# Kernel tuning notes

Measured on AMD Instinct MI355X. Metric: run time of the kernel, lower is better.

Reference implementation:

```python
import jax, jax.numpy as jnp
import numpy as np

B, S, D, H, FF = 2, 2048, 1024, 16, 4096
HD = D // H
EPS = 1e-9


def setup_inputs() -> dict:
    key = jax.random.key(0)
    ks = jax.random.split(key, 16)
    sc = 0.02
    inp = {
        "x": jax.random.normal(ks[0], (B, S, D), jnp.float32),
        "y": jax.random.normal(ks[1], (B, S, D), jnp.float32),
        "decoder_mask": jnp.tril(jnp.ones((S, S), jnp.int32))[None, None],  # [1,1,S,S]
        # self-attention params (weights stored [in,out])
        "qkv_w": jax.random.normal(ks[2], (D, 3 * D), jnp.float32) * sc,
        "qkv_b": jnp.zeros((3 * D,), jnp.float32),
        "sa_fc_w": jax.random.normal(ks[3], (D, D), jnp.float32) * sc,
        "sa_fc_b": jnp.zeros((D,), jnp.float32),
        "g1": jnp.ones((D,), jnp.float32),
        "b1": jnp.zeros((D,), jnp.float32),
        # cross-attention params
        "kv_w": jax.random.normal(ks[4], (D, 2 * D), jnp.float32) * sc,
        "kv_b": jnp.zeros((2 * D,), jnp.float32),
        "q_w": jax.random.normal(ks[5], (D, D), jnp.float32) * sc,
        "q_b": jnp.zeros((D,), jnp.float32),
        "ca_fc_w": jax.random.normal(ks[6], (D, D), jnp.float32) * sc,
        "ca_fc_b": jnp.zeros((D,), jnp.float32),
        "g2": jnp.ones((D,), jnp.float32),
        "b2": jnp.zeros((D,), jnp.float32),
        # FFN params
        "ff1_w": jax.random.normal(ks[7], (D, FF), jnp.float32) * sc,
        "ff1_b": jnp.zeros((FF,), jnp.float32),
        "ff2_w": jax.random.normal(ks[8], (FF, D), jnp.float32) * sc,
        "ff2_b": jnp.zeros((D,), jnp.float32),
        "g3": jnp.ones((D,), jnp.float32),
        "b3": jnp.zeros((D,), jnp.float32),
    }
    return inp


def _layernorm(x, g, b):
    mean = jnp.mean(x, axis=-1, keepdims=True)
    var = jnp.mean((x - mean) ** 2, axis=-1, keepdims=True)
    return g * (x - mean) / jnp.sqrt(var + EPS) + b


def _sdpa(q, k, v, mask=None):
    # q,k,v: [B,H,S,hd]
    scores = jnp.einsum("bhqd,bhkd->bhqk", q, k) / jnp.sqrt(jnp.float32(q.shape[-1]))
    if mask is not None:
        scores = jnp.where(mask == 0, jnp.float32(-1e9), scores)
    attn = jax.nn.softmax(scores, axis=-1)
    return jnp.einsum("bhqk,bhkd->bhqd", attn, v)


def reference(x, y, decoder_mask, qkv_w, qkv_b, sa_fc_w, sa_fc_b, g1, b1,
              kv_w, kv_b, q_w, q_b, ca_fc_w, ca_fc_b, g2, b2,
              ff1_w, ff1_b, ff2_w, ff2_b, g3, b3):
    b, s, d = y.shape
    # --- masked self-attention on y ---
    qkv = (y @ qkv_w + qkv_b).reshape(b, s, H, 3 * HD).transpose(0, 2, 1, 3)
    q, k, v = jnp.split(qkv, 3, axis=-1)
    vals = _sdpa(q, k, v, decoder_mask).transpose(0, 2, 1, 3).reshape(b, s, d)
    sa = vals @ sa_fc_w + sa_fc_b
    y = _layernorm(sa + y, g1, b1)
    # --- cross-attention: kv from x, q from y ---
    kv = (x @ kv_w + kv_b).reshape(b, s, H, 2 * HD).transpose(0, 2, 1, 3)
    k2, v2 = jnp.split(kv, 2, axis=-1)
    q2 = (y @ q_w + q_b).reshape(b, s, H, HD).transpose(0, 2, 1, 3)
    vals2 = _sdpa(q2, k2, v2, None).transpose(0, 2, 1, 3).reshape(b, s, d)
    ca = vals2 @ ca_fc_w + ca_fc_b
    y = _layernorm(ca + y, g2, b2)
    # --- FFN ---
    h = jax.nn.relu(y @ ff1_w + ff1_b)
    ff = h @ ff2_w + ff2_b
    y = _layernorm(ff + y, g3, b3)
    return y
```

## Files before the change

### kernel.cpp

```cpp
#include <hip/hip_runtime.h>

typedef unsigned short u16;
typedef unsigned int u32;
typedef __attribute__((ext_vector_type(4))) float f32x4;
typedef __attribute__((ext_vector_type(8))) __bf16 bf16x8;
typedef __attribute__((ext_vector_type(2))) __bf16 bf16x2;
typedef __attribute__((ext_vector_type(4))) u16 u16x4;

#define NB 2
#define NS 2048
#define ND 1024
#define NH 16
#define NHD 64
#define NFF 4096
#define NBS (NB * NS)

typedef const __attribute__((address_space(1))) unsigned int as1_u32;
typedef __attribute__((address_space(3))) unsigned int as3_u32;

__device__ __forceinline__ void gl_lds16(const u16* g, u16* l) {
  __builtin_amdgcn_global_load_lds((as1_u32*)g, (as3_u32*)l, 16, 0, 0);
}

__device__ __forceinline__ u16 f2bf(float f) {
  union { float f; unsigned u; } v; v.f = f;
  unsigned r = (v.u + 0x7FFFu + ((v.u >> 16) & 1u)) >> 16;
  return (u16)r;
}

__device__ __forceinline__ float bf2f(u16 u) {
  union { u32 u; float f; } v; v.u = ((u32)u) << 16; return v.f;
}

__device__ __forceinline__ u32 pkbf(float a, float b) {
  bf16x2 v; v[0] = (__bf16)a; v[1] = (__bf16)b;
  union { bf16x2 v; u32 u; } c; c.v = v; return c.u;
}

__device__ __forceinline__ char* lswz(void* base, int row, int bcol) {
  return (char*)base + row * 128 + (bcol ^ ((row & 7) << 4));
}
__device__ __forceinline__ const char* lswz(const void* base, int row, int bcol) {
  return (const char*)base + row * 128 + (bcol ^ ((row & 7) << 4));
}

__global__ __launch_bounds__(256) void conv_bf16(const float* __restrict__ in,
                                                 u16* __restrict__ out, int n4) {
  int i = blockIdx.x * 256 + threadIdx.x;
  if (i >= n4) return;
  f32x4 v = *reinterpret_cast<const f32x4*>(&in[(size_t)i * 4]);
  u16x4 o;
#pragma unroll
  for (int j = 0; j < 4; ++j) o[j] = f2bf(v[j]);
  *reinterpret_cast<u16x4*>(&out[(size_t)i * 4]) = o;
}

struct WSeg { const float* src; u16* dst; int N; int tile0; };
struct WAll { WSeg s[7]; };

__global__ void wconv_all(WAll wa) {
  __shared__ float t[32][33];
  int bid = blockIdx.x;
  int si = 0;
#pragma unroll
  for (int i = 1; i < 7; ++i) si += (bid >= wa.s[i].tile0) ? 1 : 0;
  const WSeg sg = wa.s[si];
  const int tt = bid - sg.tile0;
  const int tilesx = sg.N >> 5;
  const int n0 = (tt % tilesx) * 32, k0 = (tt / tilesx) * 32;
  const int K = (si == 6) ? NFF : ND;
  int tx = threadIdx.x, ty = threadIdx.y;
#pragma unroll
  for (int i = ty; i < 32; i += 8) t[i][tx] = sg.src[(size_t)(k0 + i) * sg.N + n0 + tx];
  __syncthreads();
#pragma unroll
  for (int i = ty; i < 32; i += 8)
    sg.dst[(size_t)(n0 + i) * K + k0 + tx] = f2bf(t[tx][i]);
}

template <int TM, int OUTF32, int RELU>
__global__ __launch_bounds__(256) void gemm_bt(const u16* __restrict__ A,
                                               const u16* __restrict__ BT,
                                               const float* __restrict__ bias,
                                               float* __restrict__ Cf,
                                               u16* __restrict__ Cb,
                                               int M, int N, int K) {
  constexpr int MR = TM / 32;
  constexpr int ACH = TM / 64;
  __shared__ __align__(16) u16 lA[2][TM * 32];
  __shared__ __align__(16) u16 lB[2][128 * 32];
  const int tid = threadIdx.x;
  const int lane = tid & 63, wave = tid >> 6;
  const int bm = blockIdx.y * TM, bn = blockIdx.x * 128;
  const int wr = (wave >> 1) * (MR * 16), wc = (wave & 1) * 64;
  const int r16 = lane & 15, kg = lane >> 4;

  f32x4 acc[MR][4] = {};

  auto stage = [&](int buf, int k0) {
#pragma unroll
    for (int c = 0; c < ACH; ++c) {
      int chunk = c * 256 + tid;
      int r = chunk >> 2, kc = (chunk & 3) * 8;
      gl_lds16(&A[(size_t)(bm + r) * K + k0 + kc], &lA[buf][(c * 256 + wave * 64) * 8]);
    }
#pragma unroll
    for (int c = 0; c < 2; ++c) {
      int chunk = c * 256 + tid;
      int r = chunk >> 2, kc = (chunk & 3) * 8;
      gl_lds16(&BT[(size_t)(bn + r) * K + k0 + kc], &lB[buf][(c * 256 + wave * 64) * 8]);
    }
  };

  stage(0, 0);
  __syncthreads();

  const int nk = K / 32;
  for (int i = 0; i < nk; ++i) {
    const int cur = i & 1;
    if (i + 1 < nk) stage(cur ^ 1, (i + 1) * 32);

    bf16x8 af[MR], bfr[4];
#pragma unroll
    for (int m = 0; m < MR; ++m)
      af[m] = *reinterpret_cast<const bf16x8*>(&lA[cur][(wr + m * 16 + r16) * 32 + kg * 8]);
#pragma unroll
    for (int n = 0; n < 4; ++n)
      bfr[n] = *reinterpret_cast<const bf16x8*>(&lB[cur][(wc + n * 16 + r16) * 32 + kg * 8]);
#pragma unroll
    for (int m = 0; m < MR; ++m)
#pragma unroll
      for (int n = 0; n < 4; ++n)
        acc[m][n] = __builtin_amdgcn_mfma_f32_16x16x32_bf16(af[m], bfr[n], acc[m][n], 0, 0, 0);

    __syncthreads();
  }

#pragma unroll
  for (int m = 0; m < MR; ++m) {
    int row = bm + wr + m * 16 + kg * 4;
#pragma unroll
    for (int n = 0; n < 4; ++n) {
      int col = bn + wc + n * 16 + r16;
      float bv = bias[col];
#pragma unroll
      for (int j = 0; j < 4; ++j) {
        float v = acc[m][n][j] + bv;
        if (RELU) v = fmaxf(v, 0.f);
        if (OUTF32)
          Cf[(size_t)(row + j) * N + col] = v;
        else
          Cb[(size_t)(row + j) * N + col] = f2bf(v);
      }
    }
  }
}

__global__ __launch_bounds__(256) void vt_kern(const u16* __restrict__ src, int stride,
                                               int hmul, int hadd, u16* __restrict__ VT) {
  __shared__ u16 lt[64][72];
  const int bh = blockIdx.y;
  const int b = bh >> 4, h = bh & 15;
  const int s0 = blockIdx.x * 64;
  const u16* sb = src + (size_t)b * NS * stride + h * hmul + hadd;
#pragma unroll
  for (int c = 0; c < 2; ++c) {
    int chunk = c * 256 + threadIdx.x;
    int r = chunk >> 3, d = (chunk & 7) * 8;
    *reinterpret_cast<uint4*>(&lt[r][d]) =
        *reinterpret_cast<const uint4*>(&sb[(size_t)(s0 + r) * stride + d]);
  }
  __syncthreads();
  const int d = threadIdx.x >> 2, sq = (threadIdx.x & 3) * 16;
  union { u16 e[16]; uint4 v[2]; } pk;
#pragma unroll
  for (int i = 0; i < 16; ++i) pk.e[i] = lt[sq + i][d];
  uint4* dst = reinterpret_cast<uint4*>(&VT[((size_t)bh * NHD + d) * NS + s0 + sq]);
  dst[0] = pk.v[0];
  dst[1] = pk.v[1];
}

#define C1F 0.180336880f
#define OPSZ ((size_t)32 * NS * NHD)

template <int CAUSAL>
__global__ __launch_bounds__(512) void attn10(const u16* __restrict__ Qp, int qstride,
                                              int qhm, const u16* __restrict__ Kp,
                                              int kstride, int khm, int kha,
                                              const u16* __restrict__ VT,
                                              u16* __restrict__ OP,
                                              float2* __restrict__ ML) {
  const int bid = blockIdx.x;
  const int split = blockIdx.y;
  const int xcd = bid & 7, j5 = bid >> 3;
  const int bh = xcd + 8 * (j5 >> 3);
  int qt = j5 & 7;
  if (CAUSAL) qt = 7 - qt;
  const int b = bh >> 4, h = bh & 15;
  const int tid = threadIdx.x, lane = tid & 63, wave = tid >> 6;
  const int r16 = lane & 15, kg = lane >> 4;
  const int q0w = qt * 256 + wave * 32;

  __shared__ __align__(16) char lK[2][64 * 128];
  __shared__ __align__(16) char lV[2][64 * 128];
  __shared__ __align__(16) char lP[8][16 * 128];
  char* lPw = &lP[wave][0];

  const u16* qb = Qp + (size_t)b * NS * qstride + h * qhm;
  const u16* kb = Kp + (size_t)b * NS * kstride + h * khm + kha;
  const u16* vb = VT + (size_t)bh * NHD * NS;

  const int srow = tid >> 3;
  const int sbcol = (tid & 7) * 16;
  const int scol = (tid & 7) * 8;

  bf16x8 qf[2][2];
#pragma unroll
  for (int qn = 0; qn < 2; ++qn)
#pragma unroll
    for (int ks = 0; ks < 2; ++ks) {
      bf16x8 v = *reinterpret_cast<const bf16x8*>(
          &qb[(size_t)(q0w + qn * 16 + r16) * qstride + ks * 32 + kg * 8]);
#pragma unroll
      for (int e = 0; e < 8; ++e) v[e] = (__bf16)((float)v[e] * C1F);
      qf[qn][ks] = v;
    }

  f32x4 o_acc[2][4] = {};
  float m_run[2] = {-1e30f, -1e30f}, l_lane[2] = {0.f, 0.f};

  const int ntb = CAUSAL ? (4 * qt + 4) : (NS / 64);
  const int wnt = CAUSAL ? (q0w / 64 + 1) : (NS / 64);
  const int halfb = (ntb + 1) >> 1;
  const int t0 = split ? halfb : 0;
  const int t1 = split ? ntb : halfb;

  uint4 kreg, vreg;
  auto ldregs = [&](int t) {
    const int kv0 = t * 64;
    kreg = *reinterpret_cast<const uint4*>(&kb[(size_t)(kv0 + srow) * kstride + scol]);
    vreg = *reinterpret_cast<const uint4*>(&vb[(size_t)srow * NS + kv0 + scol]);
  };
  auto wrlds = [&](int buf) {
    *reinterpret_cast<uint4*>(lswz(lK[buf], srow, sbcol)) = kreg;
    *reinterpret_cast<uint4*>(lswz(lV[buf], srow, sbcol)) = vreg;
  };

  ldregs(t0);
  wrlds(0);
  __syncthreads();

  for (int t = t0; t < t1; ++t) {
    const int cur = (t - t0) & 1;
    const bool more = (t + 1 < t1);
    if (more) ldregs(t + 1);

    if (t < wnt) {
      const int kv0 = t * 64;
      const char* lKc = lK[cur];
      const char* lVc = lV[cur];

      bf16x8 kf[8];
#pragma unroll
      for (int c = 0; c < 4; ++c)
#pragma unroll
        for (int ks = 0; ks < 2; ++ks)
          kf[c * 2 + ks] = *reinterpret_cast<const bf16x8*>(
              lswz(lKc, c * 16 + r16, ks * 64 + kg * 16));

      f32x4 s[2][4] = {};
#pragma unroll
      for (int c = 0; c < 4; ++c)
#pragma unroll
        for (int ks = 0; ks < 2; ++ks) {
          s[0][c] = __builtin_amdgcn_mfma_f32_16x16x32_bf16(kf[c * 2 + ks], qf[0][ks], s[0][c], 0, 0, 0);
          s[1][c] = __builtin_amdgcn_mfma_f32_16x16x32_bf16(kf[c * 2 + ks], qf[1][ks], s[1][c], 0, 0, 0);
        }

      bf16x8 vf[8];
#pragma unroll
      for (int cd = 0; cd < 4; ++cd)
#pragma unroll
        for (int ks = 0; ks < 2; ++ks)
          vf[cd * 2 + ks] = *reinterpret_cast<const bf16x8*>(
              lswz(lVc, cd * 16 + r16, ks * 64 + kg * 16));

#pragma unroll
      for (int qn = 0; qn < 2; ++qn) {
        if (CAUSAL && t == wnt - 1) {
          const int q = q0w + qn * 16 + r16;
#pragma unroll
          for (int c = 0; c < 4; ++c)
#pragma unroll
            for (int j = 0; j < 4; ++j)
              if (kv0 + c * 16 + kg * 4 + j > q) s[qn][c][j] = -1e31f;
        }
        float m0 = fmaxf(fmaxf(s[qn][0][0], s[qn][0][1]), fmaxf(s[qn][0][2], s[qn][0][3]));
        float m1 = fmaxf(fmaxf(s[qn][1][0], s[qn][1][1]), fmaxf(s[qn][1][2], s[qn][1][3]));
        float m2 = fmaxf(fmaxf(s[qn][2][0], s[qn][2][1]), fmaxf(s[qn][2][2], s[qn][2][3]));
        float m3 = fmaxf(fmaxf(s[qn][3][0], s[qn][3][1]), fmaxf(s[qn][3][2], s[qn][3][3]));
        float mxr = fmaxf(fmaxf(m0, m1), fmaxf(m2, m3));
        float mn = m_run[qn];
        if (!__all(mxr <= mn + 8.f)) {
          float mz = mxr;
          mz = fmaxf(mz, __shfl_xor(mz, 16));
          mz = fmaxf(mz, __shfl_xor(mz, 32));
          mn = fmaxf(m_run[qn], mz);
          const float cr = exp2f(m_run[qn] - mn);
          m_run[qn] = mn;
          l_lane[qn] *= cr;
          float crow[4];
#pragma unroll
          for (int j = 0; j < 4; ++j) crow[j] = __shfl(cr, kg * 4 + j);
#pragma unroll
          for (int cd = 0; cd < 4; ++cd)
#pragma unroll
            for (int j = 0; j < 4; ++j) o_acc[qn][cd][j] *= crow[j];
        }
        float su = 0.f;
#pragma unroll
        for (int c = 0; c < 4; ++c)
#pragma unroll
          for (int j = 0; j < 4; ++j) {
            float p = exp2f(s[qn][c][j] - mn);
            s[qn][c][j] = p;
            su += p;
          }
        l_lane[qn] += su;

#pragma unroll
        for (int c = 0; c < 4; ++c) {
          uint2 w2 = {pkbf(s[qn][c][0], s[qn][c][1]), pkbf(s[qn][c][2], s[qn][c][3])};
          *reinterpret_cast<uint2*>(lswz(lPw, r16, c * 32 + kg * 8)) = w2;
        }
        bf16x8 pf[2];
#pragma unroll
        for (int ks = 0; ks < 2; ++ks)
          pf[ks] = *reinterpret_cast<const bf16x8*>(
              lswz(lPw, r16, ks * 64 + kg * 16));
#pragma unroll
        for (int cd = 0; cd < 4; ++cd)
#pragma unroll
          for (int ks = 0; ks < 2; ++ks)
            o_acc[qn][cd] = __builtin_amdgcn_mfma_f32_16x16x32_bf16(
                pf[ks], vf[cd * 2 + ks], o_acc[qn][cd], 0, 0, 0);
      }
    }

    if (more) wrlds(cur ^ 1);
    __syncthreads();
  }

  u16* op = OP + split * OPSZ + (size_t)bh * NS * NHD;
#pragma unroll
  for (int qn = 0; qn < 2; ++qn) {
    float l = l_lane[qn];
    l += __shfl_xor(l, 16);
    l += __shfl_xor(l, 32);
#pragma unroll
    for (int cd = 0; cd < 4; ++cd) {
      int col = cd * 16 + r16;
#pragma unroll
      for (int j = 0; j < 4; ++j) {
        int row = q0w + qn * 16 + kg * 4 + j;
        op[(size_t)row * NHD + col] = f2bf(o_acc[qn][cd][j]);
      }
    }
    if (kg == 0)
      ML[(size_t)split * 32 * NS + (size_t)bh * NS + q0w + qn * 16 + r16] =
          make_float2(m_run[qn], l);
  }
}

__global__ __launch_bounds__(256) void attn_comb(const u16* __restrict__ OP,
                                                 const float2* __restrict__ ML,
                                                 u16* __restrict__ AO) {
  int idx = blockIdx.x * 256 + threadIdx.x;
  int dg = (idx & 7) * 8;
  int q = (idx >> 3) & (NS - 1);
  int bh = idx >> 14;
  int b = bh >> 4, h = bh & 15;
  float2 ml0 = ML[(size_t)bh * NS + q];
  float2 ml1 = ML[(size_t)32 * NS + (size_t)bh * NS + q];
  float M = fmaxf(ml0.x, ml1.x);
  float w0 = exp2f(ml0.x - M), w1 = exp2f(ml1.x - M);
  float linv = 1.f / (ml0.y * w0 + ml1.y * w1);
  w0 *= linv;
  w1 *= linv;
  size_t src = ((size_t)bh * NS + q) * NHD + dg;
  uint4 r0 = *reinterpret_cast<const uint4*>(&OP[src]);
  uint4 r1 = *reinterpret_cast<const uint4*>(&OP[OPSZ + src]);
  const u16* e0 = reinterpret_cast<const u16*>(&r0);
  const u16* e1 = reinterpret_cast<const u16*>(&r1);
  u16 out[8];
#pragma unroll
  for (int j = 0; j < 8; ++j)
    out[j] = f2bf(bf2f(e0[j]) * w0 + bf2f(e1[j]) * w1);
  *reinterpret_cast<uint4*>(&AO[((size_t)b * NS + q) * ND + h * NHD + dg]) =
      *reinterpret_cast<uint4*>(out);
}

__global__ __launch_bounds__(256) void ln_kern(const float* __restrict__ a,
                                               const float* __restrict__ resid,
                                               const float* __restrict__ g,
                                               const float* __restrict__ bb,
                                               float* __restrict__ outf,
                                               u16* __restrict__ outb) {
  const int row = blockIdx.x;
  const int tid = threadIdx.x;
  const size_t off = (size_t)row * ND + tid * 4;
  f32x4 v = *reinterpret_cast<const f32x4*>(&a[off]);
  f32x4 r = *reinterpret_cast<const f32x4*>(&resid[off]);
#pragma unroll
  for (int j = 0; j < 4; ++j) v[j] += r[j];
  float s = v[0] + v[1] + v[2] + v[3];
  float s2 = v[0] * v[0] + v[1] * v[1] + v[2] * v[2] + v[3] * v[3];
#pragma unroll
  for (int m = 1; m < 64; m <<= 1) {
    s += __shfl_xor(s, m);
    s2 += __shfl_xor(s2, m);
  }
  __shared__ float ws1[4], ws2[4];
  int wave = tid >> 6, lane = tid & 63;
  if (lane == 0) { ws1[wave] = s; ws2[wave] = s2; }
  __syncthreads();
  s = ws1[0] + ws1[1] + ws1[2] + ws1[3];
  s2 = ws2[0] + ws2[1] + ws2[2] + ws2[3];
  float mean = s * (1.f / ND);
  float var = fmaxf(s2 * (1.f / ND) - mean * mean, 0.f);
  float rstd = rsqrtf(var + 1e-9f);
  f32x4 gg = *reinterpret_cast<const f32x4*>(&g[tid * 4]);
  f32x4 bv = *reinterpret_cast<const f32x4*>(&bb[tid * 4]);
  f32x4 o;
  u16x4 ob;
#pragma unroll
  for (int j = 0; j < 4; ++j) {
    o[j] = gg[j] * (v[j] - mean) * rstd + bv[j];
    ob[j] = f2bf(o[j]);
  }
  *reinterpret_cast<f32x4*>(&outf[off]) = o;
  *reinterpret_cast<u16x4*>(&outb[off]) = ob;
}

extern "C" void kernel_launch(void* const* d_in, const int* in_sizes, int n_in,
                              void* d_out, int out_size, void* d_ws, size_t ws_size,
                              hipStream_t stream) {
  const float* x = (const float*)d_in[0];
  const float* y = (const float*)d_in[1];
  const float* qkv_w = (const float*)d_in[3];
  const float* qkv_b = (const float*)d_in[4];
  const float* sa_fc_w = (const float*)d_in[5];
  const float* sa_fc_b = (const float*)d_in[6];
  const float* g1 = (const float*)d_in[7];
  const float* b1 = (const float*)d_in[8];
  const float* kv_w = (const float*)d_in[9];
  const float* kv_b = (const float*)d_in[10];
  const float* q_w = (const float*)d_in[11];
  const float* q_b = (const float*)d_in[12];
  const float* ca_fc_w = (const float*)d_in[13];
  const float* ca_fc_b = (const float*)d_in[14];
  const float* g2 = (const float*)d_in[15];
  const float* b2 = (const float*)d_in[16];
  const float* ff1_w = (const float*)d_in[17];
  const float* ff1_b = (const float*)d_in[18];
  const float* ff2_w = (const float*)d_in[19];
  const float* ff2_b = (const float*)d_in[20];
  const float* g3 = (const float*)d_in[21];
  const float* b3 = (const float*)d_in[22];

  if (ws_size < (120ull << 20)) return;

  char* w = (char*)d_ws;
  u16* Wqkv = (u16*)w;
  u16* Wsa  = Wqkv + 3145728;
  u16* Wkv  = Wsa + 1048576;
  u16* Wq   = Wkv + 2097152;
  u16* Wca  = Wq + 1048576;
  u16* Wff1 = Wca + 1048576;
  u16* Wff2 = Wff1 + 4194304;
  u16* ACT = (u16*)(w + (32ull << 20));
  u16* XB  = (u16*)(w + (40ull << 20));
  u16* Qb  = (u16*)(w + (48ull << 20));
  u16* VT  = (u16*)(w + (56ull << 20));
  u16* G   = (u16*)(w + (64ull << 20));
  float* Fa = (float*)(w + (88ull << 20));
  float* Fb = (float*)(w + (104ull << 20));
  u16* H   = XB;
  u16* AO  = G;
  u16* OPb = (u16*)Fa;
  float2* ML = (float2*)ACT;
  float* OUT = (float*)d_out;

  dim3 wblk(32, 8);
  const int n4act = NBS * ND / 4;

  conv_bf16<<<n4act / 256, 256, 0, stream>>>(y, ACT, n4act);
  conv_bf16<<<n4act / 256, 256, 0, stream>>>(x, XB, n4act);
  WAll wa;
  wa.s[0] = {qkv_w, Wqkv, 3 * ND, 0};
  wa.s[1] = {sa_fc_w, Wsa, ND, 3072};
  wa.s[2] = {kv_w, Wkv, 2 * ND, 4096};
  wa.s[3] = {q_w, Wq, ND, 6144};
  wa.s[4] = {ca_fc_w, Wca, ND, 7168};
  wa.s[5] = {ff1_w, Wff1, NFF, 8192};
  wa.s[6] = {ff2_w, Wff2, ND, 12288};
  wconv_all<<<16384, wblk, 0, stream>>>(wa);

  gemm_bt<128, 0, 0><<<dim3(3 * ND / 128, NBS / 128), 256, 0, stream>>>(
      ACT, Wqkv, qkv_b, nullptr, G, NBS, 3 * ND, ND);
  vt_kern<<<dim3(NS / 64, NB * NH), 256, 0, stream>>>(G, 3 * ND, 192, 128, VT);
  attn10<1><<<dim3(256, 2), 512, 0, stream>>>(G, 3 * ND, 192, G, 3 * ND, 192, 64, VT, OPb, ML);
  attn_comb<<<2048, 256, 0, stream>>>(OPb, ML, AO);
  gemm_bt<64, 1, 0><<<dim3(ND / 128, NBS / 64), 256, 0, stream>>>(
      AO, Wsa, sa_fc_b, Fa, nullptr, NBS, ND, ND);
  ln_kern<<<NBS, 256, 0, stream>>>(Fa, y, g1, b1, Fb, ACT);

  gemm_bt<128, 0, 0><<<dim3(2 * ND / 128, NBS / 128), 256, 0, stream>>>(
      XB, Wkv, kv_b, nullptr, G, NBS, 2 * ND, ND);
  vt_kern<<<dim3(NS / 64, NB * NH), 256, 0, stream>>>(G, 2 * ND, 128, 64, VT);
  gemm_bt<64, 0, 0><<<dim3(ND / 128, NBS / 64), 256, 0, stream>>>(
      ACT, Wq, q_b, nullptr, Qb, NBS, ND, ND);
  attn10<0><<<dim3(256, 2), 512, 0, stream>>>(Qb, ND, 64, G, 2 * ND, 128, 0, VT, OPb, ML);
  attn_comb<<<2048, 256, 0, stream>>>(OPb, ML, AO);
  gemm_bt<64, 1, 0><<<dim3(ND / 128, NBS / 64), 256, 0, stream>>>(
      AO, Wca, ca_fc_b, Fa, nullptr, NBS, ND, ND);
  ln_kern<<<NBS, 256, 0, stream>>>(Fa, Fb, g2, b2, Fb, ACT);

  gemm_bt<128, 0, 1><<<dim3(NFF / 128, NBS / 128), 256, 0, stream>>>(
      ACT, Wff1, ff1_b, nullptr, H, NBS, NFF, ND);
  gemm_bt<64, 1, 0><<<dim3(ND / 128, NBS / 64), 256, 0, stream>>>(
      H, Wff2, ff2_b, Fa, nullptr, NBS, ND, NFF);
  ln_kern<<<NBS, 256, 0, stream>>>(Fa, Fb, g3, b3, OUT, ACT);
}
```

Baseline: 465.9 us.

## Fuse prep conversions, write V-transpose from GEMM epilogue, swizzle GEMM blocks

The two activation conversions and the weight-transpose conversion are merged into one launch. The GEMM epilogue now writes the transposed V directly when producing QKV/KV, which removes both vt_kern launches. GEMM workgroups are remapped so that consecutive blocks spread across XCDs for better L2 locality, and the MFMA loop raises wave priority with s_setprio. attn_comb is templated on the number of splits. The transposed-V stores are strided, 8-byte scattered writes, and the block remap changes cache behaviour.

```diff
diff --git a/kernel.cpp b/kernel.cpp
--- a/kernel.cpp
+++ b/kernel.cpp
@@ -44,32 +44,38 @@
   return (const char*)base + row * 128 + (bcol ^ ((row & 7) << 4));
 }
 
-__global__ __launch_bounds__(256) void conv_bf16(const float* __restrict__ in,
-                                                 u16* __restrict__ out, int n4) {
-  int i = blockIdx.x * 256 + threadIdx.x;
-  if (i >= n4) return;
-  f32x4 v = *reinterpret_cast<const f32x4*>(&in[(size_t)i * 4]);
-  u16x4 o;
-#pragma unroll
-  for (int j = 0; j < 4; ++j) o[j] = f2bf(v[j]);
-  *reinterpret_cast<u16x4*>(&out[(size_t)i * 4]) = o;
-}
-
 struct WSeg { const float* src; u16* dst; int N; int tile0; };
-struct WAll { WSeg s[7]; };
-
-__global__ void wconv_all(WAll wa) {
+struct PrepArgs {
+  const float* y; u16* yb;
+  const float* x; u16* xb;
+  WSeg s[7];
+};
+
+__global__ __launch_bounds__(256) void prep_all(PrepArgs pa) {
+  const int bid = blockIdx.x;
+  const int tid = threadIdx.x;
+  if (bid < 8192) {
+    const float* in = (bid < 4096) ? pa.y : pa.x;
+    u16* out = (bid < 4096) ? pa.yb : pa.xb;
+    int i = (bid & 4095) * 256 + tid;
+    f32x4 v = *reinterpret_cast<const f32x4*>(&in[(size_t)i * 4]);
+    u16x4 o;
+#pragma unroll
+    for (int j = 0; j < 4; ++j) o[j] = f2bf(v[j]);
+    *reinterpret_cast<u16x4*>(&out[(size_t)i * 4]) = o;
+    return;
+  }
   __shared__ float t[32][33];
-  int bid = blockIdx.x;
+  const int wb = bid - 8192;
   int si = 0;
 #pragma unroll
-  for (int i = 1; i < 7; ++i) si += (bid >= wa.s[i].tile0) ? 1 : 0;
-  const WSeg sg = wa.s[si];
-  const int tt = bid - sg.tile0;
+  for (int i = 1; i < 7; ++i) si += (wb >= pa.s[i].tile0) ? 1 : 0;
+  const WSeg sg = pa.s[si];
+  const int tt = wb - sg.tile0;
   const int tilesx = sg.N >> 5;
   const int n0 = (tt % tilesx) * 32, k0 = (tt / tilesx) * 32;
   const int K = (si == 6) ? NFF : ND;
-  int tx = threadIdx.x, ty = threadIdx.y;
+  const int tx = tid & 31, ty = tid >> 5;
 #pragma unroll
   for (int i = ty; i < 32; i += 8) t[i][tx] = sg.src[(size_t)(k0 + i) * sg.N + n0 + tx];
   __syncthreads();
@@ -78,12 +84,13 @@
     sg.dst[(size_t)(n0 + i) * K + k0 + tx] = f2bf(t[tx][i]);
 }
 
-template <int TM, int OUTF32, int RELU>
+template <int TM, int OUTF32, int RELU, int HM, int HA>
 __global__ __launch_bounds__(256) void gemm_bt(const u16* __restrict__ A,
                                                const u16* __restrict__ BT,
                                                const float* __restrict__ bias,
                                                float* __restrict__ Cf,
                                                u16* __restrict__ Cb,
+                                               u16* __restrict__ VTo,
                                                int M, int N, int K) {
   constexpr int MR = TM / 32;
   constexpr int ACH = TM / 64;
@@ -91,7 +98,11 @@
   __shared__ __align__(16) u16 lB[2][128 * 32];
   const int tid = threadIdx.x;
   const int lane = tid & 63, wave = tid >> 6;
-  const int bm = blockIdx.y * TM, bn = blockIdx.x * 128;
+  const u32 gx = gridDim.x;
+  const u32 nwg = gx * gridDim.y;
+  const u32 flat = blockIdx.y * gx + blockIdx.x;
+  const u32 swz = (flat & 7) * (nwg >> 3) + (flat >> 3);
+  const int bm = (swz / gx) * TM, bn = (swz % gx) * 128;
   const int wr = (wave >> 1) * (MR * 16), wc = (wave & 1) * 64;
   const int r16 = lane & 15, kg = lane >> 4;
 
@@ -127,11 +138,13 @@
 #pragma unroll
     for (int n = 0; n < 4; ++n)
       bfr[n] = *reinterpret_cast<const bf16x8*>(&lB[cur][(wc + n * 16 + r16) * 32 + kg * 8]);
+    __builtin_amdgcn_s_setprio(1);
 #pragma unroll
     for (int m = 0; m < MR; ++m)
 #pragma unroll
       for (int n = 0; n < 4; ++n)
         acc[m][n] = __builtin_amdgcn_mfma_f32_16x16x32_bf16(af[m], bfr[n], acc[m][n], 0, 0, 0);
+    __builtin_amdgcn_s_setprio(0);
 
     __syncthreads();
   }
@@ -143,41 +156,31 @@
     for (int n = 0; n < 4; ++n) {
       int col = bn + wc + n * 16 + r16;
       float bv = bias[col];
+      u16x4 ob;
 #pragma unroll
       for (int j = 0; j < 4; ++j) {
         float v = acc[m][n][j] + bv;
         if (RELU) v = fmaxf(v, 0.f);
         if (OUTF32)
           Cf[(size_t)(row + j) * N + col] = v;
-        else
-          Cb[(size_t)(row + j) * N + col] = f2bf(v);
+        else {
+          ob[j] = f2bf(v);
+          Cb[(size_t)(row + j) * N + col] = ob[j];
+        }
+      }
+      if (HM > 0) {
+        int c0 = col % HM;
+        if (c0 >= HA) {
+          int hh = col / HM;
+          int d = c0 - HA;
+          int bb = row >> 11;
+          int s = row & (NS - 1);
+          *reinterpret_cast<u16x4*>(
+              &VTo[(((size_t)(bb * NH + hh)) * NHD + d) * NS + s]) = ob;
+        }
       }
     }
   }
-}
-
-__global__ __launch_bounds__(256) void vt_kern(const u16* __restrict__ src, int stride,
-                                               int hmul, int hadd, u16* __restrict__ VT) {
-  __shared__ u16 lt[64][72];
-  const int bh = blockIdx.y;
-  const int b = bh >> 4, h = bh & 15;
-  const int s0 = blockIdx.x * 64;
-  const u16* sb = src + (size_t)b * NS * stride + h * hmul + hadd;
-#pragma unroll
-  for (int c = 0; c < 2; ++c) {
-    int chunk = c * 256 + threadIdx.x;
-    int r = chunk >> 3, d = (chunk & 7) * 8;
-    *reinterpret_cast<uint4*>(&lt[r][d]) =
-        *reinterpret_cast<const uint4*>(&sb[(size_t)(s0 + r) * stride + d]);
-  }
-  __syncthreads();
-  const int d = threadIdx.x >> 2, sq = (threadIdx.x & 3) * 16;
-  union { u16 e[16]; uint4 v[2]; } pk;
-#pragma unroll
-  for (int i = 0; i < 16; ++i) pk.e[i] = lt[sq + i][d];
-  uint4* dst = reinterpret_cast<uint4*>(&VT[((size_t)bh * NHD + d) * NS + s0 + sq]);
-  dst[0] = pk.v[0];
-  dst[1] = pk.v[1];
 }
 
 #define C1F 0.180336880f
@@ -336,8 +339,7 @@
         bf16x8 pf[2];
 #pragma unroll
         for (int ks = 0; ks < 2; ++ks)
-          pf[ks] = *reinterpret_cast<const bf16x8*>(
-              lswz(lPw, r16, ks * 64 + kg * 16));
+          pf[ks] = *reinterpret_cast<const bf16x8*>(lswz(lPw, r16, ks * 64 + kg * 16));
 #pragma unroll
         for (int cd = 0; cd < 4; ++cd)
 #pragma unroll
@@ -372,6 +374,7 @@
   }
 }
 
+template <int NSPL>
 __global__ __launch_bounds__(256) void attn_comb(const u16* __restrict__ OP,
                                                  const float2* __restrict__ ML,
                                                  u16* __restrict__ AO) {
@@ -380,22 +383,32 @@
   int q = (idx >> 3) & (NS - 1);
   int bh = idx >> 14;
   int b = bh >> 4, h = bh & 15;
-  float2 ml0 = ML[(size_t)bh * NS + q];
-  float2 ml1 = ML[(size_t)32 * NS + (size_t)bh * NS + q];
-  float M = fmaxf(ml0.x, ml1.x);
-  float w0 = exp2f(ml0.x - M), w1 = exp2f(ml1.x - M);
-  float linv = 1.f / (ml0.y * w0 + ml1.y * w1);
-  w0 *= linv;
-  w1 *= linv;
+  float2 ml[NSPL];
+  float M = -1e30f;
+#pragma unroll
+  for (int s = 0; s < NSPL; ++s) {
+    ml[s] = ML[((size_t)(s * 32 + bh)) * NS + q];
+    M = fmaxf(M, ml[s].x);
+  }
+  float wgt[NSPL], wsum = 0.f;
+#pragma unroll
+  for (int s = 0; s < NSPL; ++s) {
+    wgt[s] = exp2f(ml[s].x - M);
+    wsum += ml[s].y * wgt[s];
+  }
+  float linv = 1.f / wsum;
   size_t src = ((size_t)bh * NS + q) * NHD + dg;
-  uint4 r0 = *reinterpret_cast<const uint4*>(&OP[src]);
-  uint4 r1 = *reinterpret_cast<const uint4*>(&OP[OPSZ + src]);
-  const u16* e0 = reinterpret_cast<const u16*>(&r0);
-  const u16* e1 = reinterpret_cast<const u16*>(&r1);
+  float acc[8] = {};
+#pragma unroll
+  for (int s = 0; s < NSPL; ++s) {
+    uint4 r = *reinterpret_cast<const uint4*>(&OP[s * OPSZ + src]);
+    const u16* e = reinterpret_cast<const u16*>(&r);
+#pragma unroll
+    for (int j = 0; j < 8; ++j) acc[j] += bf2f(e[j]) * wgt[s];
+  }
   u16 out[8];
 #pragma unroll
-  for (int j = 0; j < 8; ++j)
-    out[j] = f2bf(bf2f(e0[j]) * w0 + bf2f(e1[j]) * w1);
+  for (int j = 0; j < 8; ++j) out[j] = f2bf(acc[j] * linv);
   *reinterpret_cast<uint4*>(&AO[((size_t)b * NS + q) * ND + h * NHD + dg]) =
       *reinterpret_cast<uint4*>(out);
 }
@@ -491,44 +504,38 @@
   float2* ML = (float2*)ACT;
   float* OUT = (float*)d_out;
 
-  dim3 wblk(32, 8);
-  const int n4act = NBS * ND / 4;
-
-  conv_bf16<<<n4act / 256, 256, 0, stream>>>(y, ACT, n4act);
-  conv_bf16<<<n4act / 256, 256, 0, stream>>>(x, XB, n4act);
-  WAll wa;
-  wa.s[0] = {qkv_w, Wqkv, 3 * ND, 0};
-  wa.s[1] = {sa_fc_w, Wsa, ND, 3072};
-  wa.s[2] = {kv_w, Wkv, 2 * ND, 4096};
-  wa.s[3] = {q_w, Wq, ND, 6144};
-  wa.s[4] = {ca_fc_w, Wca, ND, 7168};
-  wa.s[5] = {ff1_w, Wff1, NFF, 8192};
-  wa.s[6] = {ff2_w, Wff2, ND, 12288};
-  wconv_all<<<16384, wblk, 0, stream>>>(wa);
-
-  gemm_bt<128, 0, 0><<<dim3(3 * ND / 128, NBS / 128), 256, 0, stream>>>(
-      ACT, Wqkv, qkv_b, nullptr, G, NBS, 3 * ND, ND);
-  vt_kern<<<dim3(NS / 64, NB * NH), 256, 0, stream>>>(G, 3 * ND, 192, 128, VT);
+  PrepArgs pa;
+  pa.y = y; pa.yb = ACT; pa.x = x; pa.xb = XB;
+  pa.s[0] = {qkv_w, Wqkv, 3 * ND, 0};
+  pa.s[1] = {sa_fc_w, Wsa, ND, 3072};
+  pa.s[2] = {kv_w, Wkv, 2 * ND, 4096};
+  pa.s[3] = {q_w, Wq, ND, 6144};
+  pa.s[4] = {ca_fc_w, Wca, ND, 7168};
+  pa.s[5] = {ff1_w, Wff1, NFF, 8192};
+  pa.s[6] = {ff2_w, Wff2, ND, 12288};
+  prep_all<<<24576, 256, 0, stream>>>(pa);
+
+  gemm_bt<128, 0, 0, 192, 128><<<dim3(3 * ND / 128, NBS / 128), 256, 0, stream>>>(
+      ACT, Wqkv, qkv_b, nullptr, G, VT, NBS, 3 * ND, ND);
   attn10<1><<<dim3(256, 2), 512, 0, stream>>>(G, 3 * ND, 192, G, 3 * ND, 192, 64, VT, OPb, ML);
-  attn_comb<<<2048, 256, 0, stream>>>(OPb, ML, AO);
-  gemm_bt<64, 1, 0><<<dim3(ND / 128, NBS / 64), 256, 0, stream>>>(
-      AO, Wsa, sa_fc_b, Fa, nullptr, NBS, ND, ND);
+  attn_comb<2><<<2048, 256, 0, stream>>>(OPb, ML, AO);
+  gemm_bt<64, 1, 0, 0, 0><<<dim3(ND / 128, NBS / 64), 256, 0, stream>>>(
+      AO, Wsa, sa_fc_b, Fa, nullptr, nullptr, NBS, ND, ND);
   ln_kern<<<NBS, 256, 0, stream>>>(Fa, y, g1, b1, Fb, ACT);
 
-  gemm_bt<128, 0, 0><<<dim3(2 * ND / 128, NBS / 128), 256, 0, stream>>>(
-      XB, Wkv, kv_b, nullptr, G, NBS, 2 * ND, ND);
-  vt_kern<<<dim3(NS / 64, NB * NH), 256, 0, stream>>>(G, 2 * ND, 128, 64, VT);
-  gemm_bt<64, 0, 0><<<dim3(ND / 128, NBS / 64), 256, 0, stream>>>(
-      ACT, Wq, q_b, nullptr, Qb, NBS, ND, ND);
+  gemm_bt<128, 0, 0, 128, 64><<<dim3(2 * ND / 128, NBS / 128), 256, 0, stream>>>(
+      XB, Wkv, kv_b, nullptr, G, VT, NBS, 2 * ND, ND);
+  gemm_bt<64, 0, 0, 0, 0><<<dim3(ND / 128, NBS / 64), 256, 0, stream>>>(
+      ACT, Wq, q_b, nullptr, Qb, nullptr, NBS, ND, ND);
   attn10<0><<<dim3(256, 2), 512, 0, stream>>>(Qb, ND, 64, G, 2 * ND, 128, 0, VT, OPb, ML);
-  attn_comb<<<2048, 256, 0, stream>>>(OPb, ML, AO);
-  gemm_bt<64, 1, 0><<<dim3(ND / 128, NBS / 64), 256, 0, stream>>>(
-      AO, Wca, ca_fc_b, Fa, nullptr, NBS, ND, ND);
+  attn_comb<2><<<2048, 256, 0, stream>>>(OPb, ML, AO);
+  gemm_bt<64, 1, 0, 0, 0><<<dim3(ND / 128, NBS / 64), 256, 0, stream>>>(
+      AO, Wca, ca_fc_b, Fa, nullptr, nullptr, NBS, ND, ND);
   ln_kern<<<NBS, 256, 0, stream>>>(Fa, Fb, g2, b2, Fb, ACT);
 
-  gemm_bt<128, 0, 1><<<dim3(NFF / 128, NBS / 128), 256, 0, stream>>>(
-      ACT, Wff1, ff1_b, nullptr, H, NBS, NFF, ND);
-  gemm_bt<64, 1, 0><<<dim3(ND / 128, NBS / 64), 256, 0, stream>>>(
-      H, Wff2, ff2_b, Fa, nullptr, NBS, ND, NFF);
+  gemm_bt<128, 0, 1, 0, 0><<<dim3(NFF / 128, NBS / 128), 256, 0, stream>>>(
+      ACT, Wff1, ff1_b, nullptr, H, nullptr, NBS, NFF, ND);
+  gemm_bt<64, 1, 0, 0, 0><<<dim3(ND / 128, NBS / 64), 256, 0, stream>>>(
+      H, Wff2, ff2_b, Fa, nullptr, nullptr, NBS, ND, NFF);
   ln_kern<<<NBS, 256, 0, stream>>>(Fa, Fb, g3, b3, OUT, ACT);
 }
```

Result: faster. 450.5 us (-3.3%).
